# Optimization experiments

Measured on AMD Instinct MI355X. Metric: run time of the kernel, lower is better.

## Reference

```python
import jax, jax.numpy as jnp
import numpy as np

N = 200000      # total nodes
NG = 100000     # masked (graph) nodes
NU = N - NG     # unconnected nodes
E = 3200000     # edges (index into graph nodes)
C = 1000000     # candidate pairs


def setup_inputs() -> dict:
    key = jax.random.key(0)
    ks = jax.random.split(key, 16)
    s = 0.1  # weight init scale
    x = jax.random.normal(ks[0], (N, 2), jnp.float32)
    mask = jnp.arange(N) < NG
    candidates = jnp.stack([
        jax.random.randint(ks[1], (C,), 0, NG),
        jax.random.randint(ks[2], (C,), 0, NU),
    ], axis=1).astype(jnp.int32)
    edges = jax.random.randint(ks[3], (2, E), 0, NG).astype(jnp.int32)
    return {
        "x": x, "mask": mask, "candidates": candidates, "edges": edges,
        # GraphConv(2,8): lin_rel on aggregated neighbors, lin_root on self, bias in rel
        "w1_rel": jax.random.normal(ks[4], (2, 8), jnp.float32) * s,
        "w1_root": jax.random.normal(ks[5], (2, 8), jnp.float32) * s,
        "b1": jnp.zeros((8,), jnp.float32),
        # GraphConv(8,16)
        "w2_rel": jax.random.normal(ks[6], (8, 16), jnp.float32) * s,
        "w2_root": jax.random.normal(ks[7], (8, 16), jnp.float32) * s,
        "b2": jnp.zeros((16,), jnp.float32),
        # fc_unconnected: Linear(2,16) (source's Linear(8,16) is inconsistent with 2-dim x)
        "wu": jax.random.normal(ks[8], (2, 16), jnp.float32) * s,
        "bu": jnp.zeros((16,), jnp.float32),
        # fc: Linear(32,64) -> ReLU -> Linear(64,1)
        "wa": jax.random.normal(ks[9], (32, 64), jnp.float32) * s,
        "ba": jnp.zeros((64,), jnp.float32),
        "wb": jax.random.normal(ks[10], (64, 1), jnp.float32) * s,
        "bb": jnp.zeros((1,), jnp.float32),
    }


def graph_conv(h, edges, w_rel, w_root, b, n):
    # PyG GraphConv with aggr='add': out_i = W_rel @ sum_{j->i} h_j + W_root @ h_i + b
    src, dst = edges[0], edges[1]
    agg = jax.ops.segment_sum(h[src], dst, num_segments=n)  # [n, d_in]
    return agg @ w_rel + h @ w_root + b


def reference(x, mask, candidates, edges, w1_rel, w1_root, b1,
              w2_rel, w2_root, b2, wu, bu, wa, ba, wb, bb):
    idx_g = jnp.nonzero(mask, size=NG)[0]      # graph node indices
    idx_u = jnp.nonzero(~mask, size=NU)[0]     # unconnected node indices
    x_unconnected = x[idx_u] @ wu + bu                         # [NU, 16]
    h = jax.nn.relu(graph_conv(x[idx_g], edges, w1_rel, w1_root, b1, NG))  # [NG, 8]
    h = jax.nn.relu(graph_conv(h, edges, w2_rel, w2_root, b2, NG))         # [NG, 16]
    ec = jnp.concatenate([h[candidates[:, 0]], x_unconnected[candidates[:, 1]]], axis=-1)  # [C, 32]
    hid = jax.nn.relu(ec @ wa + ba)            # [C, 64]
    return jnp.squeeze(hid @ wb + bb, -1)      # [C]
```

## Files before the change

kernel.cpp:

```cpp
#include <hip/hip_runtime.h>

#define N_TOT  200000
#define NG_    100000
#define NU_    100000
#define E_CNT  3200000
#define C_CNT  1000000

#define NBUCK  196
#define NBLK   256
#define CHUNK  12500

#define CBLK   250
#define CCHUNK 4000

__global__ __launch_bounds__(256) void phaseA(const int* __restrict__ dst,
                                              int* __restrict__ cnt_mat) {
    __shared__ int hcnt[NBUCK];
    int t = threadIdx.x;
    if (t < NBUCK) hcnt[t] = 0;
    __syncthreads();
    int beg = blockIdx.x * CHUNK, end = beg + CHUNK;
    for (int e = beg + t; e < end; e += 256)
        atomicAdd(&hcnt[dst[e] >> 9], 1);
    __syncthreads();
    if (t < NBUCK) cnt_mat[blockIdx.x * NBUCK + t] = hcnt[t];
}

__global__ __launch_bounds__(256) void phaseB1(const int* __restrict__ cnt_mat,
                                               int* __restrict__ off_mat,
                                               int* __restrict__ colsum) {
    __shared__ int s[256];
    int t = threadIdx.x;
    int k = blockIdx.x;
    int v = cnt_mat[t * NBUCK + k];
    s[t] = v;
    __syncthreads();
    for (int off = 1; off < 256; off <<= 1) {
        int u = (t >= off) ? s[t - off] : 0;
        __syncthreads();
        s[t] += u;
        __syncthreads();
    }
    off_mat[t * NBUCK + k] = s[t] - v;
    if (t == 255) colsum[k] = s[255];
}

__global__ __launch_bounds__(256) void phaseB2(const int* __restrict__ colsum,
                                               int* __restrict__ bbase) {
    __shared__ int s[256];
    int t = threadIdx.x;
    int v = (t < NBUCK) ? colsum[t] : 0;
    s[t] = v;
    __syncthreads();
    for (int off = 1; off < 256; off <<= 1) {
        int u = (t >= off) ? s[t - off] : 0;
        __syncthreads();
        s[t] += u;
        __syncthreads();
    }
    if (t < NBUCK) bbase[t] = s[t] - v;
    if (t == NBUCK - 1) bbase[NBUCK] = s[t];
}

__global__ __launch_bounds__(256) void phaseC(const int* __restrict__ src,
                                              const int* __restrict__ dst,
                                              const int* __restrict__ off_mat,
                                              const int* __restrict__ bbase,
                                              int* __restrict__ pairs) {
    __shared__ int loc[NBUCK];
    int t = threadIdx.x;
    if (t < NBUCK) loc[t] = bbase[t] + off_mat[blockIdx.x * NBUCK + t];
    __syncthreads();
    int beg = blockIdx.x * CHUNK, end = beg + CHUNK;
    for (int e = beg + t; e < end; e += 256) {
        int d = dst[e], s = src[e];
        int k = d >> 9;
        int pos = atomicAdd(&loc[k], 1);
        pairs[pos] = (s << 9) | (d & 511);
    }
}

__global__ __launch_bounds__(1024) void phaseD(const int* __restrict__ bbase,
                                               const int* __restrict__ pairs,
                                               int* __restrict__ csr_src,
                                               int* __restrict__ node_off) {
    __shared__ int cnt[512], scn[512], base[512];
    int t = threadIdx.x, k = blockIdx.x;
    if (t < 512) cnt[t] = 0;
    __syncthreads();
    int beg = bbase[k], end = bbase[k + 1];
    for (int e = beg + t; e < end; e += 1024)
        atomicAdd(&cnt[pairs[e] & 511], 1);
    __syncthreads();
    if (t < 512) scn[t] = cnt[t];
    __syncthreads();
    for (int off = 1; off < 512; off <<= 1) {
        int v = 0;
        if (t < 512 && t >= off) v = scn[t - off];
        __syncthreads();
        if (t < 512) scn[t] += v;
        __syncthreads();
    }
    if (t < 512) {
        int bse = beg + scn[t] - cnt[t];
        base[t] = bse;
        node_off[(k << 9) + t] = bse;
    }
    __syncthreads();
    for (int e = beg + t; e < end; e += 1024) {
        int p = pairs[e];
        int pos = atomicAdd(&base[p & 511], 1);
        csr_src[pos] = p >> 9;
    }
}

__global__ __launch_bounds__(256) void conv1_csr(const int* __restrict__ node_off,
                                                 const int* __restrict__ csr_src,
                                                 const float* __restrict__ x,
                                                 const float* __restrict__ w_rel,
                                                 const float* __restrict__ w_root,
                                                 const float* __restrict__ b,
                                                 float* __restrict__ h1) {
    int t = threadIdx.x;
    int n = blockIdx.x * 32 + (t >> 3);
    int l = t & 7;
    int beg = node_off[n], end = node_off[n + 1];
    float a0 = 0.f, a1 = 0.f;
    for (int e = beg + l; e < end; e += 8) {
        int s = csr_src[e];
        float2 xv = *(const float2*)(x + 2 * s);
        a0 += xv.x; a1 += xv.y;
    }
#pragma unroll
    for (int d = 1; d < 8; d <<= 1) {
        a0 += __shfl_xor(a0, d, 64);
        a1 += __shfl_xor(a1, d, 64);
    }
    float2 xn = *(const float2*)(x + 2 * n);
    float v = a0 * w_rel[l] + a1 * w_rel[8 + l]
            + xn.x * w_root[l] + xn.y * w_root[8 + l] + b[l];
    h1[8 * n + l] = fmaxf(v, 0.f);
}

__global__ __launch_bounds__(256) void conv2_csr(const int* __restrict__ node_off,
                                                 const int* __restrict__ csr_src,
                                                 const float* __restrict__ h1,
                                                 const float* __restrict__ w_rel,
                                                 const float* __restrict__ w_root,
                                                 const float* __restrict__ b,
                                                 float* __restrict__ h2) {
    int t = threadIdx.x;
    int n = blockIdx.x * 32 + (t >> 3);
    int l = t & 7;
    int beg = node_off[n], end = node_off[n + 1];
    float acc[8] = {0.f, 0.f, 0.f, 0.f, 0.f, 0.f, 0.f, 0.f};
    for (int e = beg + l; e < end; e += 8) {
        int s = csr_src[e];
        const float4* hp = (const float4*)(h1 + 8 * s);
        float4 v0 = hp[0], v1 = hp[1];
        acc[0] += v0.x; acc[1] += v0.y; acc[2] += v0.z; acc[3] += v0.w;
        acc[4] += v1.x; acc[5] += v1.y; acc[6] += v1.z; acc[7] += v1.w;
    }
#pragma unroll
    for (int d = 1; d < 8; d <<= 1)
#pragma unroll
        for (int j = 0; j < 8; j++)
            acc[j] += __shfl_xor(acc[j], d, 64);
    const float4* hp = (const float4*)(h1 + 8 * n);
    float4 t0 = hp[0], t1 = hp[1];
    float hn[8] = {t0.x, t0.y, t0.z, t0.w, t1.x, t1.y, t1.z, t1.w};
#pragma unroll
    for (int cc = 0; cc < 2; cc++) {
        int c = l + 8 * cc;
        float v = b[c];
#pragma unroll
        for (int j = 0; j < 8; j++)
            v += acc[j] * w_rel[j * 16 + c] + hn[j] * w_root[j * 16 + c];
        h2[16 * n + c] = fmaxf(v, 0.f);
    }
}

__global__ void prep_kernel(const float* __restrict__ wu,
                            const float* __restrict__ bu,
                            const float* __restrict__ wa,
                            const float* __restrict__ ba,
                            float* __restrict__ wprep) {
    int j = threadIdx.x;
#pragma unroll
    for (int i = 0; i < 16; i++) wprep[j * 16 + i] = wa[i * 64 + j];
    float c0 = 0.f, c1 = 0.f, bc = ba[j];
#pragma unroll
    for (int k = 0; k < 16; k++) {
        float w = wa[(16 + k) * 64 + j];
        c0 += wu[k] * w;
        c1 += wu[16 + k] * w;
        bc += bu[k] * w;
    }
    wprep[1024 + j] = c0;
    wprep[1088 + j] = c1;
    wprep[1152 + j] = bc;
}

__global__ __launch_bounds__(256) void precompA(const float* __restrict__ h2,
                                                const float* __restrict__ wa,
                                                const float* __restrict__ wprep,
                                                float* __restrict__ Ag) {
    int g = blockIdx.x * 256 + threadIdx.x;
    if (g >= NG_) return;
    float h[16];
    const float4* hp = (const float4*)(h2 + 16 * g);
#pragma unroll
    for (int q = 0; q < 4; q++) {
        float4 v = hp[q];
        h[4*q] = v.x; h[4*q+1] = v.y; h[4*q+2] = v.z; h[4*q+3] = v.w;
    }
    float4* op = (float4*)(Ag + 64 * g);
#pragma unroll
    for (int q = 0; q < 16; q++) {
        float4 v;
        v.x = wprep[1152 + 4*q + 0];
        v.y = wprep[1152 + 4*q + 1];
        v.z = wprep[1152 + 4*q + 2];
        v.w = wprep[1152 + 4*q + 3];
#pragma unroll
        for (int i = 0; i < 16; i++) {
            float hi = h[i];
            v.x += hi * wa[i*64 + 4*q + 0];
            v.y += hi * wa[i*64 + 4*q + 1];
            v.z += hi * wa[i*64 + 4*q + 2];
            v.w += hi * wa[i*64 + 4*q + 3];
        }
        op[q] = v;
    }
}

__global__ __launch_bounds__(256) void candA(const int* __restrict__ cand,
                                             int* __restrict__ cnt2) {
    __shared__ int hcnt[NBUCK];
    int t = threadIdx.x;
    if (t < NBUCK) hcnt[t] = 0;
    __syncthreads();
    int beg = blockIdx.x * CCHUNK, end = beg + CCHUNK;
    for (int e = beg + t; e < end; e += 256)
        atomicAdd(&hcnt[cand[2 * e] >> 9], 1);
    __syncthreads();
    if (t < NBUCK) cnt2[blockIdx.x * NBUCK + t] = hcnt[t];
}

__global__ __launch_bounds__(256) void candB1(const int* __restrict__ cnt2,
                                              int* __restrict__ off2,
                                              int* __restrict__ csum2) {
    __shared__ int s[256];
    int t = threadIdx.x;
    int k = blockIdx.x;
    int v = (t < CBLK) ? cnt2[t * NBUCK + k] : 0;
    s[t] = v;
    __syncthreads();
    for (int off = 1; off < 256; off <<= 1) {
        int u = (t >= off) ? s[t - off] : 0;
        __syncthreads();
        s[t] += u;
        __syncthreads();
    }
    if (t < CBLK) off2[t * NBUCK + k] = s[t] - v;
    if (t == 255) csum2[k] = s[255];
}

__global__ __launch_bounds__(256) void candB2(const int* __restrict__ csum2,
                                              int* __restrict__ bbase2) {
    __shared__ int s[256];
    int t = threadIdx.x;
    int v = (t < NBUCK) ? csum2[t] : 0;
    s[t] = v;
    __syncthreads();
    for (int off = 1; off < 256; off <<= 1) {
        int u = (t >= off) ? s[t - off] : 0;
        __syncthreads();
        s[t] += u;
        __syncthreads();
    }
    if (t < NBUCK) bbase2[t] = s[t] - v;
    if (t == NBUCK - 1) bbase2[NBUCK] = s[t];
}

__global__ __launch_bounds__(256) void candC(const int* __restrict__ cand,
                                             const int* __restrict__ off2,
                                             const int* __restrict__ bbase2,
                                             int2* __restrict__ sc) {
    __shared__ int loc[NBUCK];
    int t = threadIdx.x;
    if (t < NBUCK) loc[t] = bbase2[t] + off2[blockIdx.x * NBUCK + t];
    __syncthreads();
    int beg = blockIdx.x * CCHUNK, end = beg + CCHUNK;
    for (int e = beg + t; e < end; e += 256) {
        int g = cand[2 * e], u = cand[2 * e + 1];
        int k = g >> 9;
        int pos = atomicAdd(&loc[k], 1);
        int w0 = g | (u << 17);
        int w1 = (int)(((unsigned)u >> 15) | ((unsigned)e << 2));
        sc[pos] = make_int2(w0, w1);
    }
}

__global__ __launch_bounds__(256) void final_mlp5(const int2* __restrict__ sc,
                                                  const float* __restrict__ Ag,
                                                  const float* __restrict__ x,
                                                  const float* __restrict__ wprep,
                                                  const float* __restrict__ wb,
                                                  const float* __restrict__ bb,
                                                  float* __restrict__ out) {
    int nwg = gridDim.x;
    int xcd = blockIdx.x & 7, pos = blockIdx.x >> 3;
    int q = nwg >> 3, r = nwg & 7;
    int wg = (xcd < r ? xcd * (q + 1) : r * (q + 1) + (xcd - r) * q) + pos;

    int c = wg * 256 + threadIdx.x;
    if (c >= C_CNT) return;
    int2 w = sc[c];
    unsigned w0 = (unsigned)w.x, w1 = (unsigned)w.y;
    int g   = (int)(w0 & 0x1FFFFu);
    int u   = (int)((w0 >> 17) | ((w1 & 3u) << 15));
    int idx = (int)(w1 >> 2);
    float2 xv = *(const float2*)(x + 2 * (NG_ + u));
    const float4* ap = (const float4*)(Ag + 64 * g);
    float acc = bb[0];
#pragma unroll
    for (int qq = 0; qq < 16; qq++) {
        float4 a = ap[qq];
        float v0 = a.x + xv.x * wprep[1024 + 4*qq + 0] + xv.y * wprep[1088 + 4*qq + 0];
        float v1 = a.y + xv.x * wprep[1024 + 4*qq + 1] + xv.y * wprep[1088 + 4*qq + 1];
        float v2 = a.z + xv.x * wprep[1024 + 4*qq + 2] + xv.y * wprep[1088 + 4*qq + 2];
        float v3 = a.w + xv.x * wprep[1024 + 4*qq + 3] + xv.y * wprep[1088 + 4*qq + 3];
        acc += fmaxf(v0, 0.f) * wb[4*qq + 0];
        acc += fmaxf(v1, 0.f) * wb[4*qq + 1];
        acc += fmaxf(v2, 0.f) * wb[4*qq + 2];
        acc += fmaxf(v3, 0.f) * wb[4*qq + 3];
    }
    out[idx] = acc;
}


extern "C" void kernel_launch(void* const* d_in, const int* in_sizes, int n_in,
                              void* d_out, int out_size, void* d_ws, size_t ws_size,
                              hipStream_t stream) {
    const float* x      = (const float*)d_in[0];
    const int*   cand   = (const int*)d_in[2];
    const int*   edges  = (const int*)d_in[3];
    const float* w1_rel = (const float*)d_in[4];
    const float* w1_root= (const float*)d_in[5];
    const float* b1     = (const float*)d_in[6];
    const float* w2_rel = (const float*)d_in[7];
    const float* w2_root= (const float*)d_in[8];
    const float* b2     = (const float*)d_in[9];
    const float* wu     = (const float*)d_in[10];
    const float* bu     = (const float*)d_in[11];
    const float* wa     = (const float*)d_in[12];
    const float* ba     = (const float*)d_in[13];
    const float* wb     = (const float*)d_in[14];
    const float* bb     = (const float*)d_in[15];
    float* out = (float*)d_out;

    const int* src = edges;
    const int* dst = edges + E_CNT;

    int* ws_i = (int*)d_ws;
    int*   cnt_mat  = ws_i;
    int*   off_mat  = ws_i + 50176;
    int*   colsum   = ws_i + 100352;
    int*   bbase    = ws_i + 100608;
    int*   node_off = ws_i + 100864;
    float* wprep    = (float*)(ws_i + 201728);
    int*   pairs    = ws_i + 202944;
    int*   csr_src  = ws_i + 3402944;
    float* h1       = (float*)(ws_i + 6602944);
    float* h2       = (float*)(ws_i + 7402944);
    float* Ag       = (float*)(ws_i + 202944);
    int*   cnt2     = ws_i;
    int*   off2     = ws_i + 50176;
    int*   csum2    = ws_i + 100352;
    int*   bbase2   = ws_i + 100608;
    int2*  sc       = (int2*)(ws_i + 6602944);

    dim3 blk256(256);

    prep_kernel<<<1, 64, 0, stream>>>(wu, bu, wa, ba, wprep);
    phaseA <<<NBLK, blk256, 0, stream>>>(dst, cnt_mat);
    phaseB1<<<NBUCK, blk256, 0, stream>>>(cnt_mat, off_mat, colsum);
    phaseB2<<<1, blk256, 0, stream>>>(colsum, bbase);
    phaseC <<<NBLK, blk256, 0, stream>>>(src, dst, off_mat, bbase, pairs);
    phaseD <<<NBUCK, 1024, 0, stream>>>(bbase, pairs, csr_src, node_off);
    conv1_csr<<<3125, blk256, 0, stream>>>(node_off, csr_src, x, w1_rel, w1_root, b1, h1);
    conv2_csr<<<3125, blk256, 0, stream>>>(node_off, csr_src, h1, w2_rel, w2_root, b2, h2);
    precompA<<<(NG_ + 255) / 256, blk256, 0, stream>>>(h2, wa, wprep, Ag);
    candA <<<CBLK, blk256, 0, stream>>>(cand, cnt2);
    candB1<<<NBUCK, blk256, 0, stream>>>(cnt2, off2, csum2);
    candB2<<<1, blk256, 0, stream>>>(csum2, bbase2);
    candC <<<CBLK, blk256, 0, stream>>>(cand, off2, bbase2, sc);
    final_mlp5<<<(C_CNT + 255) / 256, blk256, 0, stream>>>(sc, Ag, x, wprep, wb, bb, out);
}
```

Before: 296.3 us.

## Fuse candidate bucket-sort passes into edge CSR build kernels with extended workspace

Merges the candidate histogram, scan and scatter passes into the matching edge-sorting kernels (phaseA/B1/B2/C), and folds the weight prep into the second scan kernel. This cuts the kernel launch count from fourteen to nine and overlaps candidate sorting with edge sorting. Because the candidate buffers can no longer alias the edge buffers, they move to a separate workspace region, and the fused path is used only when the workspace is large enough. The final MLP kernel also issues all sixteen Ag row loads before computing, to raise memory-level parallelism at the cost of more registers.

```diff
diff --git a/kernel.cpp b/kernel.cpp
--- a/kernel.cpp
+++ b/kernel.cpp
@@ -12,6 +12,143 @@
 
 #define CBLK   250
 #define CCHUNK 4000
+#define CCH_E  3907
+
+
+__global__ __launch_bounds__(256) void phaseA_f(const int* __restrict__ dst,
+                                                const int* __restrict__ cand,
+                                                int* __restrict__ cnt_mat,
+                                                int* __restrict__ cnt2) {
+    __shared__ int hcnt[NBUCK];
+    int t = threadIdx.x;
+    if (t < NBUCK) hcnt[t] = 0;
+    __syncthreads();
+    int beg = blockIdx.x * CHUNK, end = beg + CHUNK;
+    for (int e = beg + t; e < end; e += 256)
+        atomicAdd(&hcnt[dst[e] >> 9], 1);
+    __syncthreads();
+    if (t < NBUCK) { cnt_mat[blockIdx.x * NBUCK + t] = hcnt[t]; hcnt[t] = 0; }
+    __syncthreads();
+    int cbeg = blockIdx.x * CCH_E;
+    int cend = min(cbeg + CCH_E, C_CNT);
+    for (int e = cbeg + t; e < cend; e += 256)
+        atomicAdd(&hcnt[cand[2 * e] >> 9], 1);
+    __syncthreads();
+    if (t < NBUCK) cnt2[blockIdx.x * NBUCK + t] = hcnt[t];
+}
+
+__global__ __launch_bounds__(256) void phaseB1_f(const int* __restrict__ cnt_mat,
+                                                 const int* __restrict__ cnt2,
+                                                 int* __restrict__ off_mat,
+                                                 int* __restrict__ off2,
+                                                 int* __restrict__ colsum,
+                                                 int* __restrict__ csum2) {
+    __shared__ int s[256];
+    int t = threadIdx.x;
+    int k = blockIdx.x % NBUCK;
+    bool is_cand = blockIdx.x >= NBUCK;
+    const int* cm = is_cand ? cnt2 : cnt_mat;
+    int v = cm[t * NBUCK + k];
+    s[t] = v;
+    __syncthreads();
+    for (int off = 1; off < 256; off <<= 1) {
+        int u = (t >= off) ? s[t - off] : 0;
+        __syncthreads();
+        s[t] += u;
+        __syncthreads();
+    }
+    int* om = is_cand ? off2 : off_mat;
+    om[t * NBUCK + k] = s[t] - v;
+    if (t == 255) (is_cand ? csum2 : colsum)[k] = s[255];
+}
+
+__global__ __launch_bounds__(256) void phaseB2_f(const int* __restrict__ colsum,
+                                                 const int* __restrict__ csum2,
+                                                 int* __restrict__ bbase,
+                                                 int* __restrict__ bbase2,
+                                                 const float* __restrict__ wu,
+                                                 const float* __restrict__ bu,
+                                                 const float* __restrict__ wa,
+                                                 const float* __restrict__ ba,
+                                                 float* __restrict__ wprep) {
+    __shared__ int s[256];
+    int t = threadIdx.x;
+    int v = (t < NBUCK) ? colsum[t] : 0;
+    s[t] = v;
+    __syncthreads();
+    for (int off = 1; off < 256; off <<= 1) {
+        int u = (t >= off) ? s[t - off] : 0;
+        __syncthreads();
+        s[t] += u;
+        __syncthreads();
+    }
+    if (t < NBUCK) bbase[t] = s[t] - v;
+    if (t == NBUCK - 1) bbase[NBUCK] = s[t];
+    __syncthreads();
+    int v2 = (t < NBUCK) ? csum2[t] : 0;
+    s[t] = v2;
+    __syncthreads();
+    for (int off = 1; off < 256; off <<= 1) {
+        int u = (t >= off) ? s[t - off] : 0;
+        __syncthreads();
+        s[t] += u;
+        __syncthreads();
+    }
+    if (t < NBUCK) bbase2[t] = s[t] - v2;
+    if (t == NBUCK - 1) bbase2[NBUCK] = s[t];
+    if (t < 64) {
+        int j = t;
+#pragma unroll
+        for (int i = 0; i < 16; i++) wprep[j * 16 + i] = wa[i * 64 + j];
+        float c0 = 0.f, c1 = 0.f, bc = ba[j];
+#pragma unroll
+        for (int k2 = 0; k2 < 16; k2++) {
+            float w = wa[(16 + k2) * 64 + j];
+            c0 += wu[k2] * w;
+            c1 += wu[16 + k2] * w;
+            bc += bu[k2] * w;
+        }
+        wprep[1024 + j] = c0;
+        wprep[1088 + j] = c1;
+        wprep[1152 + j] = bc;
+    }
+}
+
+__global__ __launch_bounds__(256) void phaseC_f(const int* __restrict__ src,
+                                                const int* __restrict__ dst,
+                                                const int* __restrict__ off_mat,
+                                                const int* __restrict__ bbase,
+                                                const int* __restrict__ cand,
+                                                const int* __restrict__ off2,
+                                                const int* __restrict__ bbase2,
+                                                int* __restrict__ pairs,
+                                                int2* __restrict__ sc) {
+    __shared__ int loc[NBUCK];
+    int t = threadIdx.x;
+    if (t < NBUCK) loc[t] = bbase[t] + off_mat[blockIdx.x * NBUCK + t];
+    __syncthreads();
+    int beg = blockIdx.x * CHUNK, end = beg + CHUNK;
+    for (int e = beg + t; e < end; e += 256) {
+        int d = dst[e], s = src[e];
+        int k = d >> 9;
+        int pos = atomicAdd(&loc[k], 1);
+        pairs[pos] = (s << 9) | (d & 511);
+    }
+    __syncthreads();
+    if (t < NBUCK) loc[t] = bbase2[t] + off2[blockIdx.x * NBUCK + t];
+    __syncthreads();
+    int cbeg = blockIdx.x * CCH_E;
+    int cend = min(cbeg + CCH_E, C_CNT);
+    for (int e = cbeg + t; e < cend; e += 256) {
+        int g = cand[2 * e], u = cand[2 * e + 1];
+        int k = g >> 9;
+        int pos = atomicAdd(&loc[k], 1);
+        int w0 = g | (u << 17);
+        int w1 = (int)(((unsigned)u >> 15) | ((unsigned)e << 2));
+        sc[pos] = make_int2(w0, w1);
+    }
+}
+
 
 __global__ __launch_bounds__(256) void phaseA(const int* __restrict__ dst,
                                               int* __restrict__ cnt_mat) {
@@ -79,6 +216,96 @@
         pairs[pos] = (s << 9) | (d & 511);
     }
 }
+
+__global__ void prep_kernel(const float* __restrict__ wu,
+                            const float* __restrict__ bu,
+                            const float* __restrict__ wa,
+                            const float* __restrict__ ba,
+                            float* __restrict__ wprep) {
+    int j = threadIdx.x;
+#pragma unroll
+    for (int i = 0; i < 16; i++) wprep[j * 16 + i] = wa[i * 64 + j];
+    float c0 = 0.f, c1 = 0.f, bc = ba[j];
+#pragma unroll
+    for (int k = 0; k < 16; k++) {
+        float w = wa[(16 + k) * 64 + j];
+        c0 += wu[k] * w;
+        c1 += wu[16 + k] * w;
+        bc += bu[k] * w;
+    }
+    wprep[1024 + j] = c0;
+    wprep[1088 + j] = c1;
+    wprep[1152 + j] = bc;
+}
+
+__global__ __launch_bounds__(256) void candA(const int* __restrict__ cand,
+                                             int* __restrict__ cnt2) {
+    __shared__ int hcnt[NBUCK];
+    int t = threadIdx.x;
+    if (t < NBUCK) hcnt[t] = 0;
+    __syncthreads();
+    int beg = blockIdx.x * CCHUNK, end = beg + CCHUNK;
+    for (int e = beg + t; e < end; e += 256)
+        atomicAdd(&hcnt[cand[2 * e] >> 9], 1);
+    __syncthreads();
+    if (t < NBUCK) cnt2[blockIdx.x * NBUCK + t] = hcnt[t];
+}
+
+__global__ __launch_bounds__(256) void candB1(const int* __restrict__ cnt2,
+                                              int* __restrict__ off2,
+                                              int* __restrict__ csum2) {
+    __shared__ int s[256];
+    int t = threadIdx.x;
+    int k = blockIdx.x;
+    int v = (t < CBLK) ? cnt2[t * NBUCK + k] : 0;
+    s[t] = v;
+    __syncthreads();
+    for (int off = 1; off < 256; off <<= 1) {
+        int u = (t >= off) ? s[t - off] : 0;
+        __syncthreads();
+        s[t] += u;
+        __syncthreads();
+    }
+    if (t < CBLK) off2[t * NBUCK + k] = s[t] - v;
+    if (t == 255) csum2[k] = s[255];
+}
+
+__global__ __launch_bounds__(256) void candB2(const int* __restrict__ csum2,
+                                              int* __restrict__ bbase2) {
+    __shared__ int s[256];
+    int t = threadIdx.x;
+    int v = (t < NBUCK) ? csum2[t] : 0;
+    s[t] = v;
+    __syncthreads();
+    for (int off = 1; off < 256; off <<= 1) {
+        int u = (t >= off) ? s[t - off] : 0;
+        __syncthreads();
+        s[t] += u;
+        __syncthreads();
+    }
+    if (t < NBUCK) bbase2[t] = s[t] - v;
+    if (t == NBUCK - 1) bbase2[NBUCK] = s[t];
+}
+
+__global__ __launch_bounds__(256) void candC(const int* __restrict__ cand,
+                                             const int* __restrict__ off2,
+                                             const int* __restrict__ bbase2,
+                                             int2* __restrict__ sc) {
+    __shared__ int loc[NBUCK];
+    int t = threadIdx.x;
+    if (t < NBUCK) loc[t] = bbase2[t] + off2[blockIdx.x * NBUCK + t];
+    __syncthreads();
+    int beg = blockIdx.x * CCHUNK, end = beg + CCHUNK;
+    for (int e = beg + t; e < end; e += 256) {
+        int g = cand[2 * e], u = cand[2 * e + 1];
+        int k = g >> 9;
+        int pos = atomicAdd(&loc[k], 1);
+        int w0 = g | (u << 17);
+        int w1 = (int)(((unsigned)u >> 15) | ((unsigned)e << 2));
+        sc[pos] = make_int2(w0, w1);
+    }
+}
+
 
 __global__ __launch_bounds__(1024) void phaseD(const int* __restrict__ bbase,
                                                const int* __restrict__ pairs,
@@ -180,27 +407,6 @@
     }
 }
 
-__global__ void prep_kernel(const float* __restrict__ wu,
-                            const float* __restrict__ bu,
-                            const float* __restrict__ wa,
-                            const float* __restrict__ ba,
-                            float* __restrict__ wprep) {
-    int j = threadIdx.x;
-#pragma unroll
-    for (int i = 0; i < 16; i++) wprep[j * 16 + i] = wa[i * 64 + j];
-    float c0 = 0.f, c1 = 0.f, bc = ba[j];
-#pragma unroll
-    for (int k = 0; k < 16; k++) {
-        float w = wa[(16 + k) * 64 + j];
-        c0 += wu[k] * w;
-        c1 += wu[16 + k] * w;
-        bc += bu[k] * w;
-    }
-    wprep[1024 + j] = c0;
-    wprep[1088 + j] = c1;
-    wprep[1152 + j] = bc;
-}
-
 __global__ __launch_bounds__(256) void precompA(const float* __restrict__ h2,
                                                 const float* __restrict__ wa,
                                                 const float* __restrict__ wprep,
@@ -234,75 +440,7 @@
     }
 }
 
-__global__ __launch_bounds__(256) void candA(const int* __restrict__ cand,
-                                             int* __restrict__ cnt2) {
-    __shared__ int hcnt[NBUCK];
-    int t = threadIdx.x;
-    if (t < NBUCK) hcnt[t] = 0;
-    __syncthreads();
-    int beg = blockIdx.x * CCHUNK, end = beg + CCHUNK;
-    for (int e = beg + t; e < end; e += 256)
-        atomicAdd(&hcnt[cand[2 * e] >> 9], 1);
-    __syncthreads();
-    if (t < NBUCK) cnt2[blockIdx.x * NBUCK + t] = hcnt[t];
-}
-
-__global__ __launch_bounds__(256) void candB1(const int* __restrict__ cnt2,
-                                              int* __restrict__ off2,
-                                              int* __restrict__ csum2) {
-    __shared__ int s[256];
-    int t = threadIdx.x;
-    int k = blockIdx.x;
-    int v = (t < CBLK) ? cnt2[t * NBUCK + k] : 0;
-    s[t] = v;
-    __syncthreads();
-    for (int off = 1; off < 256; off <<= 1) {
-        int u = (t >= off) ? s[t - off] : 0;
-        __syncthreads();
-        s[t] += u;
-        __syncthreads();
-    }
-    if (t < CBLK) off2[t * NBUCK + k] = s[t] - v;
-    if (t == 255) csum2[k] = s[255];
-}
-
-__global__ __launch_bounds__(256) void candB2(const int* __restrict__ csum2,
-                                              int* __restrict__ bbase2) {
-    __shared__ int s[256];
-    int t = threadIdx.x;
-    int v = (t < NBUCK) ? csum2[t] : 0;
-    s[t] = v;
-    __syncthreads();
-    for (int off = 1; off < 256; off <<= 1) {
-        int u = (t >= off) ? s[t - off] : 0;
-        __syncthreads();
-        s[t] += u;
-        __syncthreads();
-    }
-    if (t < NBUCK) bbase2[t] = s[t] - v;
-    if (t == NBUCK - 1) bbase2[NBUCK] = s[t];
-}
-
-__global__ __launch_bounds__(256) void candC(const int* __restrict__ cand,
-                                             const int* __restrict__ off2,
-                                             const int* __restrict__ bbase2,
-                                             int2* __restrict__ sc) {
-    __shared__ int loc[NBUCK];
-    int t = threadIdx.x;
-    if (t < NBUCK) loc[t] = bbase2[t] + off2[blockIdx.x * NBUCK + t];
-    __syncthreads();
-    int beg = blockIdx.x * CCHUNK, end = beg + CCHUNK;
-    for (int e = beg + t; e < end; e += 256) {
-        int g = cand[2 * e], u = cand[2 * e + 1];
-        int k = g >> 9;
-        int pos = atomicAdd(&loc[k], 1);
-        int w0 = g | (u << 17);
-        int w1 = (int)(((unsigned)u >> 15) | ((unsigned)e << 2));
-        sc[pos] = make_int2(w0, w1);
-    }
-}
-
-__global__ __launch_bounds__(256) void final_mlp5(const int2* __restrict__ sc,
+__global__ __launch_bounds__(256) void final_mlp6(const int2* __restrict__ sc,
                                                   const float* __restrict__ Ag,
                                                   const float* __restrict__ x,
                                                   const float* __restrict__ wprep,
@@ -323,10 +461,13 @@
     int idx = (int)(w1 >> 2);
     float2 xv = *(const float2*)(x + 2 * (NG_ + u));
     const float4* ap = (const float4*)(Ag + 64 * g);
+    float4 rr[16];
+#pragma unroll
+    for (int qq = 0; qq < 16; qq++) rr[qq] = ap[qq];
     float acc = bb[0];
 #pragma unroll
     for (int qq = 0; qq < 16; qq++) {
-        float4 a = ap[qq];
+        float4 a = rr[qq];
         float v0 = a.x + xv.x * wprep[1024 + 4*qq + 0] + xv.y * wprep[1088 + 4*qq + 0];
         float v1 = a.y + xv.x * wprep[1024 + 4*qq + 1] + xv.y * wprep[1088 + 4*qq + 1];
         float v2 = a.z + xv.x * wprep[1024 + 4*qq + 2] + xv.y * wprep[1088 + 4*qq + 2];
@@ -375,26 +516,50 @@
     float* h1       = (float*)(ws_i + 6602944);
     float* h2       = (float*)(ws_i + 7402944);
     float* Ag       = (float*)(ws_i + 202944);
-    int*   cnt2     = ws_i;
-    int*   off2     = ws_i + 50176;
-    int*   csum2    = ws_i + 100352;
-    int*   bbase2   = ws_i + 100608;
-    int2*  sc       = (int2*)(ws_i + 6602944);
+
+    bool ext = ws_size >= (size_t)11103808 * sizeof(int);
 
     dim3 blk256(256);
 
-    prep_kernel<<<1, 64, 0, stream>>>(wu, bu, wa, ba, wprep);
-    phaseA <<<NBLK, blk256, 0, stream>>>(dst, cnt_mat);
-    phaseB1<<<NBUCK, blk256, 0, stream>>>(cnt_mat, off_mat, colsum);
-    phaseB2<<<1, blk256, 0, stream>>>(colsum, bbase);
-    phaseC <<<NBLK, blk256, 0, stream>>>(src, dst, off_mat, bbase, pairs);
-    phaseD <<<NBUCK, 1024, 0, stream>>>(bbase, pairs, csr_src, node_off);
-    conv1_csr<<<3125, blk256, 0, stream>>>(node_off, csr_src, x, w1_rel, w1_root, b1, h1);
-    conv2_csr<<<3125, blk256, 0, stream>>>(node_off, csr_src, h1, w2_rel, w2_root, b2, h2);
-    precompA<<<(NG_ + 255) / 256, blk256, 0, stream>>>(h2, wa, wprep, Ag);
-    candA <<<CBLK, blk256, 0, stream>>>(cand, cnt2);
-    candB1<<<NBUCK, blk256, 0, stream>>>(cnt2, off2, csum2);
-    candB2<<<1, blk256, 0, stream>>>(csum2, bbase2);
-    candC <<<CBLK, blk256, 0, stream>>>(cand, off2, bbase2, sc);
-    final_mlp5<<<(C_CNT + 255) / 256, blk256, 0, stream>>>(sc, Ag, x, wprep, wb, bb, out);
-}
+    if (ext) {
+        int*  cnt2   = ws_i + 9002944;
+        int*  off2   = ws_i + 9053120;
+        int*  csum2  = ws_i + 9103296;
+        int*  bbase2 = ws_i + 9103552;
+        int2* sc     = (int2*)(ws_i + 9103808);
+
+        phaseA_f <<<NBLK, blk256, 0, stream>>>(dst, cand, cnt_mat, cnt2);
+        phaseB1_f<<<2 * NBUCK, blk256, 0, stream>>>(cnt_mat, cnt2, off_mat, off2,
+                                                    colsum, csum2);
+        phaseB2_f<<<1, blk256, 0, stream>>>(colsum, csum2, bbase, bbase2,
+                                            wu, bu, wa, ba, wprep);
+        phaseC_f <<<NBLK, blk256, 0, stream>>>(src, dst, off_mat, bbase,
+                                               cand, off2, bbase2, pairs, sc);
+        phaseD <<<NBUCK, 1024, 0, stream>>>(bbase, pairs, csr_src, node_off);
+        conv1_csr<<<3125, blk256, 0, stream>>>(node_off, csr_src, x, w1_rel, w1_root, b1, h1);
+        conv2_csr<<<3125, blk256, 0, stream>>>(node_off, csr_src, h1, w2_rel, w2_root, b2, h2);
+        precompA<<<(NG_ + 255) / 256, blk256, 0, stream>>>(h2, wa, wprep, Ag);
+        final_mlp6<<<(C_CNT + 255) / 256, blk256, 0, stream>>>(sc, Ag, x, wprep, wb, bb, out);
+    } else {
+        int*  cnt2   = ws_i;
+        int*  off2   = ws_i + 50176;
+        int*  csum2  = ws_i + 100352;
+        int*  bbase2 = ws_i + 100608;
+        int2* sc     = (int2*)(ws_i + 6602944);
+
+        prep_kernel<<<1, 64, 0, stream>>>(wu, bu, wa, ba, wprep);
+        phaseA <<<NBLK, blk256, 0, stream>>>(dst, cnt_mat);
+        phaseB1<<<NBUCK, blk256, 0, stream>>>(cnt_mat, off_mat, colsum);
+        phaseB2<<<1, blk256, 0, stream>>>(colsum, bbase);
+        phaseC <<<NBLK, blk256, 0, stream>>>(src, dst, off_mat, bbase, pairs);
+        phaseD <<<NBUCK, 1024, 0, stream>>>(bbase, pairs, csr_src, node_off);
+        conv1_csr<<<3125, blk256, 0, stream>>>(node_off, csr_src, x, w1_rel, w1_root, b1, h1);
+        conv2_csr<<<3125, blk256, 0, stream>>>(node_off, csr_src, h1, w2_rel, w2_root, b2, h2);
+        precompA<<<(NG_ + 255) / 256, blk256, 0, stream>>>(h2, wa, wprep, Ag);
+        candA <<<CBLK, blk256, 0, stream>>>(cand, cnt2);
+        candB1<<<NBUCK, blk256, 0, stream>>>(cnt2, off2, csum2);
+        candB2<<<1, blk256, 0, stream>>>(csum2, bbase2);
+        candC <<<CBLK, blk256, 0, stream>>>(cand, off2, bbase2, sc);
+        final_mlp6<<<(C_CNT + 255) / 256, blk256, 0, stream>>>(sc, Ag, x, wprep, wb, bb, out);
+    }
+}
```

Measured after the change: 291.1 us. No clear change (-1.8%).
